# Kernel optimization log

Hardware: AMD Instinct MI355X
Metric: run time of the kernel (lower is better)

## Reference

```python
import jax, jax.numpy as jnp
import numpy as np

IMG_SIZE = 224
ALPHA = 100.0  # hardcoded softmax temperature in knnsearch_t_grad


def _sqdist(a, b):
    # (B,N,C),(B,M,C) -> (B,N,M) squared euclidean distances
    return (jnp.sum(a * a, -1)[:, :, None]
            - 2.0 * jnp.einsum('bnc,bmc->bnm', a, b)
            + jnp.sum(b * b, -1)[:, None, :])


def _cdist(a, b):
    return jnp.sqrt(jnp.maximum(_sqdist(a, b), 1e-12))


def proj2img(pc, img_offset):
    # faithful jax port of GraphDeformLoss_Neural_Partial.proj2img
    B, N, _ = pc.shape
    pc_max = pc.max(axis=1)              # (B,3)
    pc_min_full = pc.min(axis=1)         # (B,3)
    pc_range = pc_max - pc_min_full
    grid_size = pc_range[:, :2].max(axis=-1) / (IMG_SIZE - 3)   # (B,)
    pc_min = pc_min_full[:, None, :2]                            # (B,1,2)
    gs = grid_size[:, None, None]
    idx_xy = jnp.floor((pc[:, :, :2] - pc_min) / gs)             # (B,N,2)
    # densify each point into a 5x5 neighborhood of pixels
    idx_dense = (idx_xy[:, :, None, :] + img_offset[None, None]).reshape(B, N * 25, 2) + 1.0
    center = jnp.floor((idx_dense.max(axis=1) + idx_dense.min(axis=1)) / 2.0)  # (B,2)
    offset = IMG_SIZE / 2.0 - center - 1.0                       # (B,2) = (offset_x, offset_y)
    idx_off = idx_dense + offset[:, None, :]
    # boundary correction as in the torch code, plus clip for safety
    idx_off = idx_off + (idx_off < 0).astype(jnp.float32) - (idx_off > IMG_SIZE - 1).astype(jnp.float32)
    idx_off = jnp.clip(idx_off, 0, IMG_SIZE - 1)
    f_dense = jnp.repeat(jnp.repeat(pc[:, :, None, 2:3], 25, axis=2).reshape(B, N * 25, 1), 3, axis=-1)
    flat = (idx_off[..., 0] * IMG_SIZE + idx_off[..., 1]).astype(jnp.int32)   # (B,N*25)
    out = jax.vmap(lambda f, i: jax.ops.segment_sum(f, i, num_segments=IMG_SIZE * IMG_SIZE))(f_dense, flat)
    img = out.reshape(B, IMG_SIZE, IMG_SIZE, 3).transpose(0, 3, 1, 2)  # (B,3,H,W)
    return jax.nn.sigmoid(img)


def setup_inputs() -> dict:
    key = jax.random.key(0)
    k1, k2, k3, k4 = jax.random.split(key, 4)
    B, N, M, C = 4, 4995, 4995, 128
    off = jnp.array([[i, j] for i in range(-2, 3) for j in range(-2, 3)], dtype=jnp.float32)
    return {
        'verts1': jax.random.normal(k1, (B, N, 3), jnp.float32),
        'verts2': jax.random.normal(k2, (B, M, 3), jnp.float32),
        'feat1': jax.random.normal(k3, (B, N, C), jnp.float32),
        'feat2': jax.random.normal(k4, (B, M, C), jnp.float32),
        'img_offset': off,
        'k': 10,
    }


def reference(verts1, verts2, feat1, feat2, img_offset, k):
    # knnsearch_t_grad: soft correspondence from feature-space cdist + softmax
    d_feat = _cdist(feat1, feat2)                               # (B,N,M)
    Pi_12 = jax.nn.softmax(-ALPHA * d_feat, axis=-1)
    verts12 = jnp.einsum('bnm,bmc->bnc', Pi_12, verts2)         # pulled-back points (B,N,3)
    # chamfer (squared distances, as chamfer_3DDist); partial: take dist1 branch (N<=M)
    d2 = _sqdist(verts12, verts2)
    self_rec_loss = jnp.mean(jnp.min(d2, axis=-1))
    # knn_grad + index_points: gather k-NN features on source cloud
    d2_11 = _sqdist(verts1, verts1)
    _, idx11 = jax.lax.top_k(-d2_11, k)                         # (B,N,k) nearest
    feat1_conv = jax.vmap(lambda p, i: p[i])(feat1, idx11)      # (B,N,k,C)
    deform_feat_loss = jnp.mean((feat1_conv - feat1[:, :, None, :]) ** 2)
    # point-to-image projection loss
    img1 = proj2img(verts12, img_offset)
    img2 = proj2img(verts2, img_offset)
    img_loss = jnp.mean((img1 - img2) ** 2)
    return self_rec_loss + img_loss + deform_feat_loss
```

## Files before the change

### kernel.cpp

```cpp
#include <hip/hip_runtime.h>
#include <math.h>

#define BB 4
#define NN 4995
#define CC 128
#define IMG 224
#define IMGP (IMG*IMG)
#define ALPHA_F 100.0f
#define SPLITS 8
#define COLS_PER_SPLIT 640
#define RBLK 40
#define NG 158
#define NCP 5120
#define NTAP (2*BB*NN*25)
#define NREP 4
#define TKCAP 256

#define SM_SCALE 20813.6898f
#define NEG2S   -41627.3796f
#define EPS_S    2.08136898e-8f

#define OFF_V12    0
#define OFF_FN1    60000
#define OFF_V1Q    81000
#define OFF_V2Q    161000
#define OFF_C2Q    241000
#define OFF_PART   323000
#define OFF_IMG1   1123000
#define OFF_IMG2   1323704
#define OFF_ACC    1524408
#define OFF_STATS  1524792
#define OFF_F2H    1525000
#define OFF_F2L    2820000
#define OFF_IMGR   4115000
#define WS_NEED_REP ((size_t)5721000*sizeof(float))
#define ZERO_START OFF_IMG1
#define ZERO_FLOATS (1524920 - OFF_IMG1)

typedef short v8s  __attribute__((ext_vector_type(8)));
typedef float v16f __attribute__((ext_vector_type(16)));

#if __has_builtin(__builtin_amdgcn_exp2f)
__device__ __forceinline__ float fast_exp2(float x){ return __builtin_amdgcn_exp2f(x); }
#else
__device__ __forceinline__ float fast_exp2(float x){ float r; asm("v_exp_f32 %0, %1" : "=v"(r) : "v"(x)); return r; }
#endif
#if __has_builtin(__builtin_amdgcn_sqrtf)
__device__ __forceinline__ float fast_sqrt(float x){ return __builtin_amdgcn_sqrtf(x); }
#else
__device__ __forceinline__ float fast_sqrt(float x){ float r; asm("v_sqrt_f32 %0, %1" : "=v"(r) : "v"(x)); return r; }
#endif

__device__ __forceinline__ float wave_min(float v){
#pragma unroll
  for (int off=32; off; off>>=1) v = fminf(v, __shfl_xor(v, off));
  return v;
}
__device__ __forceinline__ float wave_sum(float v){
#pragma unroll
  for (int off=32; off; off>>=1) v += __shfl_xor(v, off);
  return v;
}

__device__ __forceinline__ int pack_bf_hi(float a, float b){
  return (int)__builtin_amdgcn_perm(__float_as_uint(b), __float_as_uint(a), 0x07060302u);
}

__device__ __forceinline__ void cvt_hilo(float4 a, float4 c, int4& hi, int4& lo){
  float hx=__uint_as_float(__float_as_uint(a.x)&0xffff0000u);
  float hy=__uint_as_float(__float_as_uint(a.y)&0xffff0000u);
  float hz=__uint_as_float(__float_as_uint(a.z)&0xffff0000u);
  float hw=__uint_as_float(__float_as_uint(a.w)&0xffff0000u);
  float gx=__uint_as_float(__float_as_uint(c.x)&0xffff0000u);
  float gy=__uint_as_float(__float_as_uint(c.y)&0xffff0000u);
  float gz=__uint_as_float(__float_as_uint(c.z)&0xffff0000u);
  float gw=__uint_as_float(__float_as_uint(c.w)&0xffff0000u);
  hi = make_int4(pack_bf_hi(a.x,a.y), pack_bf_hi(a.z,a.w),
                 pack_bf_hi(c.x,c.y), pack_bf_hi(c.z,c.w));
  lo = make_int4(pack_bf_hi(a.x-hx,a.y-hy), pack_bf_hi(a.z-hz,a.w-hw),
                 pack_bf_hi(c.x-gx,c.y-gy), pack_bf_hi(c.z-gz,c.w-gw));
}

__device__ __forceinline__ v8s i4_to_s8(int4 v){
  union { int4 i; v8s s; } u; u.i = v; return u.s;
}

__device__ __forceinline__ void gld_lds16(const void* g, void* l){
  __builtin_amdgcn_global_load_lds((const __attribute__((address_space(1))) void*)g,
                                   (__attribute__((address_space(3))) void*)l, 16, 0, 0);
}

__device__ __forceinline__ unsigned int fkey(float f){
  unsigned int u = __float_as_uint(f);
  return ((int)u < 0) ? ~u : (u ^ 0x80000000u);
}

__global__ __launch_bounds__(256) void k_norms(const float* __restrict__ verts1, const float* __restrict__ verts2,
                        const float* __restrict__ feat1, const float* __restrict__ feat2,
                        float* __restrict__ ws) {
  int gt = blockIdx.x*blockDim.x + threadIdx.x;
  int i = gt >> 2, sub = gt & 3;
  if (i >= BB*NCP) return;
  int b = i / NCP, col = i - b*NCP;
  if (col >= NN){
    if (sub == 0)
      ((float4*)(ws+OFF_C2Q))[i] = make_float4(0.f,0.f,0.f,1e30f);
    return;
  }
  int r = b*NN + col;
  const float4* fa = (const float4*)(feat1 + (size_t)r*CC) + sub*8;
  const float4* fb = (const float4*)(feat2 + (size_t)r*CC) + sub*8;
  float s1=0.f, s2=0.f;
#pragma unroll
  for (int k=0;k<8;k++){
    float4 t = fa[k];
    s1 = fmaf(t.x,t.x,s1); s1 = fmaf(t.y,t.y,s1); s1 = fmaf(t.z,t.z,s1); s1 = fmaf(t.w,t.w,s1);
    float4 u = fb[k];
    s2 = fmaf(u.x,u.x,s2); s2 = fmaf(u.y,u.y,s2); s2 = fmaf(u.z,u.z,s2); s2 = fmaf(u.w,u.w,s2);
  }
  s1 += __shfl_xor(s1,1); s1 += __shfl_xor(s1,2);
  s2 += __shfl_xor(s2,1); s2 += __shfl_xor(s2,2);
  if (sub == 0){
    float x=verts1[(size_t)r*3], y=verts1[(size_t)r*3+1], z=verts1[(size_t)r*3+2];
    ((float4*)(ws+OFF_V1Q))[r] = make_float4(x,y,z, x*x+y*y+z*z);
    float x2=verts2[(size_t)r*3], y2=verts2[(size_t)r*3+1], z2=verts2[(size_t)r*3+2];
    ((float4*)(ws+OFF_V2Q))[r] = make_float4(x2,y2,z2, x2*x2+y2*y2+z2*z2);
    ((float4*)(ws+OFF_C2Q))[i] = make_float4(x2,y2,z2, SM_SCALE*s2);
    ws[OFF_FN1+r] = SM_SCALE*s1;
  }
}

__global__ __launch_bounds__(256) void k_conv(const float* __restrict__ feat2, float* __restrict__ ws) {
  int g = blockIdx.x, b = blockIdx.y;
  int t = threadIdx.x;
  int q = t >> 5, c32 = t & 31;
  int col = g*32 + c32; if (col > NN-1) col = NN-1;
  const float4* src = (const float4*)(feat2 + ((size_t)(b*NN + col))*CC) + q*4;
  float4 v0 = src[0], v1 = src[1], v2 = src[2], v3 = src[3];
  short* f2h = (short*)(ws + OFF_F2H);
  short* f2l = (short*)(ws + OFF_F2L);
  size_t base = ((size_t)(b*NG + g))*4096 + (size_t)q*512 + c32*8;
  int4 hi, lo;
  cvt_hilo(v0, v1, hi, lo);
  *(int4*)&f2h[base] = hi;  *(int4*)&f2l[base] = lo;
  cvt_hilo(v2, v3, hi, lo);
  *(int4*)&f2h[base + 256] = hi;  *(int4*)&f2l[base + 256] = lo;
}

__global__ __launch_bounds__(256) void k_stageA(const float* __restrict__ feat1,
      float* __restrict__ ws) {
  __shared__ __align__(16) short Bbuf[2][4096];

  int rblk  = blockIdx.x;
  int split = blockIdx.y;
  int b     = blockIdx.z;
  int rowBase = rblk*128;
  int colBase = split*COLS_PER_SPLIT;
  int colEnd  = colBase + COLS_PER_SPLIT; if (colEnd > NN) colEnd = NN;
  int nct = (colEnd - colBase + 63) >> 6;
  int nst = nct << 2;

  int t    = threadIdx.x;
  int w    = t >> 6;
  int lane = t & 63;
  int half = lane >> 5;
  int m32  = lane & 31;

  const float* f1b = feat1 + (size_t)b*NN*CC;
  const short* f2h = (const short*)(ws + OFF_F2H);
  const short* f2l = (const short*)(ws + OFF_F2L);
  const float4* cq = (const float4*)(ws + OFF_C2Q) + (size_t)b*NCP + colBase;

  size_t f2base = (((size_t)(b*NG) + (colBase>>5) + (w>>1)) << 12) + (size_t)((t&127)*8);

  {
    short* d = &Bbuf[0][0] + w*512;
    gld_lds16(f2h + f2base, d);
    gld_lds16(f2l + f2base, d + 2048);
  }

  int nrow = rowBase + w*32 + m32;
  int nclamp = nrow > NN-1 ? NN-1 : nrow;
  float sn = ws[OFF_FN1 + (size_t)b*NN + nclamp];
  const float4* ar = (const float4*)(f1b + (size_t)nclamp*CC) + (half<<1);
  v8s Afh[8], Afl[8];
#pragma unroll
  for (int sl=0; sl<8; ++sl){
    float4 v0 = ar[sl*4], v1 = ar[sl*4+1];
    int4 hi, lo;
    cvt_hilo(v0, v1, hi, lo);
    Afh[sl] = i4_to_s8(hi); Afl[sl] = i4_to_s8(lo);
  }

  __syncthreads();

  float mm = INFINITY, S = 0.f, Vx = 0.f, Vy = 0.f, Vz = 0.f;

  for (int ci = 0; ci < nct; ci++){
    v16f acc0, acc1;
#pragma unroll
    for (int i=0;i<16;i++){ acc0[i]=0.f; acc1[i]=0.f; }

#pragma unroll
    for (int kt = 0; kt < 4; kt++){
      int s = (ci<<2) + kt;
      if (s+1 < nst){
        int s1 = s+1;
        size_t so = f2base + ((size_t)(s1>>2)<<13) + ((size_t)(s1&3)<<10);
        short* d = &Bbuf[0][0] + ((s1&1)<<12) + w*512;
        gld_lds16(f2h + so, d);
        gld_lds16(f2l + so, d + 2048);
      }
      const short* Bh = &Bbuf[0][0] + ((s&1)<<12);
      const short* Bl = Bh + 2048;
#pragma unroll
      for (int kh=0; kh<2; kh++){
        int fo = (kh<<9) + (half<<8) + (m32<<3);
        v8s a0h = *(const v8s*)&Bh[fo];
        v8s a0l = *(const v8s*)&Bl[fo];
        v8s a1h = *(const v8s*)&Bh[1024+fo];
        v8s a1l = *(const v8s*)&Bl[1024+fo];
        v8s b1h = Afh[kt*2+kh];
        v8s b1l = Afl[kt*2+kh];
        __builtin_amdgcn_s_setprio(1);
        acc0 = __builtin_amdgcn_mfma_f32_32x32x16_bf16(a0h, b1h, acc0, 0,0,0);
        acc0 = __builtin_amdgcn_mfma_f32_32x32x16_bf16(a0h, b1l, acc0, 0,0,0);
        acc0 = __builtin_amdgcn_mfma_f32_32x32x16_bf16(a0l, b1h, acc0, 0,0,0);
        acc1 = __builtin_amdgcn_mfma_f32_32x32x16_bf16(a1h, b1h, acc1, 0,0,0);
        acc1 = __builtin_amdgcn_mfma_f32_32x32x16_bf16(a1h, b1l, acc1, 0,0,0);
        acc1 = __builtin_amdgcn_mfma_f32_32x32x16_bf16(a1l, b1h, acc1, 0,0,0);
        __builtin_amdgcn_s_setprio(0);
      }
      __syncthreads();
    }

    const float4* cqt = cq + (ci<<6) + (half<<2);
    const float* cqf = (const float*)cqt;
    float Mt = INFINITY;
#pragma unroll
    for (int reg=0; reg<16; reg++){
      int idx = (reg&3) + 8*(reg>>2);
      float f0 = cqf[idx*4 + 3];
      float d0 = fmaf(NEG2S, acc0[reg], sn) + f0;
      float p0 = fast_sqrt(fmaxf(d0, EPS_S));
      acc0[reg] = p0; Mt = fminf(Mt, p0);
      float f1v = cqf[(idx+32)*4 + 3];
      float d1 = fmaf(NEG2S, acc1[reg], sn) + f1v;
      float p1 = fast_sqrt(fmaxf(d1, EPS_S));
      acc1[reg] = p1; Mt = fminf(Mt, p1);
    }
    float mn = fminf(mm, Mt);
    float sc = fast_exp2(mn - mm);
    float se=0.f, sx=0.f, sy=0.f, sz=0.f;
#pragma unroll
    for (int reg=0; reg<16; reg++){
      int idx = (reg&3) + 8*(reg>>2);
      float4 q0 = cqt[idx];
      float e0 = fast_exp2(mn - acc0[reg]);
      se += e0; sx=fmaf(e0,q0.x,sx); sy=fmaf(e0,q0.y,sy); sz=fmaf(e0,q0.z,sz);
      float4 q1 = cqt[idx+32];
      float e1 = fast_exp2(mn - acc1[reg]);
      se += e1; sx=fmaf(e1,q1.x,sx); sy=fmaf(e1,q1.y,sy); sz=fmaf(e1,q1.z,sz);
    }
    S  = fmaf(S,  sc, se);
    Vx = fmaf(Vx, sc, sx);
    Vy = fmaf(Vy, sc, sy);
    Vz = fmaf(Vz, sc, sz);
    mm = mn;
  }

  {
    float m2  = __shfl_xor(mm, 32);
    float S2  = __shfl_xor(S,  32);
    float Vx2 = __shfl_xor(Vx, 32);
    float Vy2 = __shfl_xor(Vy, 32);
    float Vz2 = __shfl_xor(Vz, 32);
    float M = fminf(mm, m2);
    float c1 = fast_exp2(M - mm), c2 = fast_exp2(M - m2);
    float Sf  = S*c1  + S2*c2;
    float Vxf = Vx*c1 + Vx2*c2;
    float Vyf = Vy*c1 + Vy2*c2;
    float Vzf = Vz*c1 + Vz2*c2;
    if (half==0 && nrow < NN){
      float* p = ws + OFF_PART + ((size_t)(b*NN+nrow)*SPLITS + split)*5;
      p[0]=M; p[1]=Sf; p[2]=Vxf; p[3]=Vyf; p[4]=Vzf;
    }
  }
}

__global__ void k_combine(float* __restrict__ ws) {
  int row = blockIdx.x*blockDim.x + threadIdx.x;
  if (row >= BB*NN) return;
  const float* p = ws + OFF_PART + (size_t)row*SPLITS*5;
  float mm = INFINITY;
#pragma unroll
  for (int s=0;s<SPLITS;s++) mm = fminf(mm, p[s*5]);
  float S=0.f,Vx=0.f,Vy=0.f,Vz=0.f;
#pragma unroll
  for (int s=0;s<SPLITS;s++){
    float sc = fast_exp2(mm - p[s*5]);
    S  += p[s*5+1]*sc; Vx += p[s*5+2]*sc; Vy += p[s*5+3]*sc; Vz += p[s*5+4]*sc;
  }
  ws[OFF_V12+(size_t)row*3+0]=Vx/S;
  ws[OFF_V12+(size_t)row*3+1]=Vy/S;
  ws[OFF_V12+(size_t)row*3+2]=Vz/S;
}

__global__ __launch_bounds__(256) void k_selfrec(float* __restrict__ ws) {
  int rblk = blockIdx.x, b = blockIdx.y;
  int lane = threadIdx.x & 63, w = threadIdx.x >> 6;
  int r0 = rblk*32 + w*8;
  const float4* v2q = (const float4*)(ws + OFF_V2Q) + (size_t)b*NN;
  const float* v12 = ws + OFF_V12 + (size_t)b*NN*3;
  float xr[8], yr[8], zr[8], sar[8]; bool val[8];
#pragma unroll
  for (int j=0;j<8;j++){
    int n = r0+j; val[j] = (n < NN); int nc = val[j] ? n : NN-1;
    float x=v12[(size_t)nc*3], y=v12[(size_t)nc*3+1], z=v12[(size_t)nc*3+2];
    sar[j]=x*x+y*y+z*z;
    xr[j]=-2.0f*x; yr[j]=-2.0f*y; zr[j]=-2.0f*z;
  }
  float mn[8];
#pragma unroll
  for (int j=0;j<8;j++) mn[j] = INFINITY;
  for (int m=lane; m<NN; m+=64) {
    float4 q = v2q[m];
#pragma unroll
    for (int j=0;j<8;j++)
      mn[j] = fminf(mn[j], fmaf(xr[j],q.x, fmaf(yr[j],q.y, fmaf(zr[j],q.z, q.w))));
  }
  float s = 0.f;
#pragma unroll
  for (int j=0;j<8;j++){
    float v = wave_min(mn[j]);
    s += val[j] ? (v + sar[j]) : 0.f;
  }
  if (lane==0)
    atomicAdd(((double*)(ws+OFF_ACC)) + ((rblk*4 + w) & 63), (double)s);
}

__global__ __launch_bounds__(256, 4) void k_topk(const float* __restrict__ feat1,
        const int* __restrict__ kptr, float* __restrict__ ws) {
  __shared__ unsigned int keybuf[4*256];
  __shared__ unsigned long long cand[4*TKCAP];
  __shared__ int scnt[4];
  __shared__ float tfs[4];
  __shared__ int sel[4][16];
  __shared__ float rs[4];
  int t = threadIdx.x;
  int lane = t & 63, wid = t >> 6;
  int b = blockIdx.y;
  int n0 = blockIdx.x*4;
  int kk = *kptr; if (kk > 16) kk = 16; if (kk < 1) kk = 1;

  const float4* v1q = (const float4*)(ws + OFF_V1Q) + (size_t)b*NN;
  float mx[4], my2[4], mz[4];
#pragma unroll
  for (int j=0;j<4;j++){
    int n = n0+j; if (n > NN-1) n = NN-1;
    float4 me = v1q[n];
    mx[j]=-2.0f*me.x; my2[j]=-2.0f*me.y; mz[j]=-2.0f*me.z;
  }
  if (t < 4) scnt[t] = 0;

  float e2[20][4];
  float mn[4] = {INFINITY, INFINITY, INFINITY, INFINITY};
#pragma unroll
  for (int i=0;i<19;i++){
    int m = t + 256*i;
    float4 q = v1q[m];
#pragma unroll
    for (int j=0;j<4;j++){
      float d = fmaf(mx[j], q.x, fmaf(my2[j], q.y, fmaf(mz[j], q.z, q.w)));
      e2[i][j] = d; mn[j] = fminf(mn[j], d);
    }
  }
  {
    int m = t + 256*19;
    bool ok = (m < NN);
    float4 q = v1q[ok ? m : NN-1];
#pragma unroll
    for (int j=0;j<4;j++){
      float d = fmaf(mx[j], q.x, fmaf(my2[j], q.y, fmaf(mz[j], q.z, q.w)));
      d = ok ? d : 1e30f;
      e2[19][j] = d; mn[j] = fminf(mn[j], d);
    }
  }

#pragma unroll
  for (int j=0;j<4;j++)
    keybuf[j*256 + t] = fkey(mn[j]) >> 16;
  __syncthreads();

  {
    unsigned int k0 = keybuf[wid*256 + lane];
    unsigned int k1 = keybuf[wid*256 + 64 + lane];
    unsigned int k2 = keybuf[wid*256 + 128 + lane];
    unsigned int k3 = keybuf[wid*256 + 192 + lane];
    unsigned int prefix = 0;
    for (int bit=15; bit>=0; --bit){
      unsigned int piv = prefix | (1u<<bit);
      int c = __popcll(__ballot(k0 < piv)) + __popcll(__ballot(k1 < piv))
            + __popcll(__ballot(k2 < piv)) + __popcll(__ballot(k3 < piv));
      if (c < kk) prefix = piv;
    }
    unsigned int K = (prefix<<16) | 0xFFFFu;
    unsigned int fb = (K & 0x80000000u) ? (K ^ 0x80000000u) : ~K;
    if (lane==0) tfs[wid] = __uint_as_float(fb);
  }
  __syncthreads();
  float tff[4] = {tfs[0], tfs[1], tfs[2], tfs[3]};

#pragma unroll
  for (int i=0;i<20;i++){
    int m = t + 256*i;
#pragma unroll
    for (int j=0;j<4;j++){
      if (e2[i][j] <= tff[j]){
        int pos = atomicAdd(&scnt[j], 1);
        if (pos < TKCAP)
          cand[j*TKCAP + pos] = ((unsigned long long)fkey(e2[i][j]) << 13) | (unsigned int)m;
      }
    }
  }
  __syncthreads();

  {
    int cnt = scnt[wid]; if (cnt > TKCAP) cnt = TKCAP;
    unsigned long long kv0 = (lane       < cnt) ? cand[wid*TKCAP + lane]       : ~0ull;
    unsigned long long kv1 = (lane + 64  < cnt) ? cand[wid*TKCAP + lane + 64]  : ~0ull;
    unsigned long long kv2 = (lane + 128 < cnt) ? cand[wid*TKCAP + lane + 128] : ~0ull;
    unsigned long long kv3 = (lane + 192 < cnt) ? cand[wid*TKCAP + lane + 192] : ~0ull;
    int r0=0, r1=0, r2=0, r3=0;
    for (int q2=0; q2<cnt; ++q2){
      unsigned long long cj = cand[wid*TKCAP + q2];
      r0 += (cj < kv0); r1 += (cj < kv1); r2 += (cj < kv2); r3 += (cj < kv3);
    }
    if (lane       < cnt && r0 < kk) sel[wid][r0] = (int)(kv0 & 8191ull);
    if (lane + 64  < cnt && r1 < kk) sel[wid][r1] = (int)(kv1 & 8191ull);
    if (lane + 128 < cnt && r2 < kk) sel[wid][r2] = (int)(kv2 & 8191ull);
    if (lane + 192 < cnt && r3 < kk) sel[wid][r3] = (int)(kv3 & 8191ull);
  }
  __syncthreads();

  float mse = 0.f;
  int c = t & 127;
  int rh = t >> 7;
  for (int j=0;j<4;j++){
    int n = n0+j;
    if (n >= NN) break;
    const float* f1n = feat1 + ((size_t)b*NN + n)*CC;
    float e = f1n[c];
    for (int r=rh; r<kk; r+=2){
      const float* g = feat1 + ((size_t)b*NN + sel[j][r])*CC;
      float d = g[c]-e;
      mse = fmaf(d,d,mse);
    }
  }

  float acc = wave_sum(mse);
  if (lane==0) rs[wid] = acc;
  __syncthreads();
  if (t==0){
    float s = (rs[0]+rs[1])+(rs[2]+rs[3]);
    atomicAdd(((double*)(ws+OFF_ACC)) + 128 + ((blockIdx.x + b) & 63), (double)s);
  }
}

__global__ void k_imgstats(const float* __restrict__ verts2, const float* __restrict__ imgoff,
                           float* __restrict__ ws) {
  __shared__ float r0[4], r1[4], r2[4], r3[4];
  __shared__ float sgs, smnx, smny;
  int img = blockIdx.x >> 2, b = blockIdx.x & 3;
  const float* pc = (img==0) ? (ws + OFF_V12 + (size_t)b*NN*3) : (verts2 + (size_t)b*NN*3);
  int lane = threadIdx.x & 63, wid = threadIdx.x >> 6;
  float mnx=INFINITY, mxx=-INFINITY, mny=INFINITY, mxy=-INFINITY;
  for (int n = threadIdx.x; n < NN; n += 256) {
    float x = pc[(size_t)n*3], y = pc[(size_t)n*3+1];
    mnx=fminf(mnx,x); mxx=fmaxf(mxx,x); mny=fminf(mny,y); mxy=fmaxf(mxy,y);
  }
#pragma unroll
  for (int off=32; off; off>>=1) {
    mnx=fminf(mnx,__shfl_xor(mnx,off)); mxx=fmaxf(mxx,__shfl_xor(mxx,off));
    mny=fminf(mny,__shfl_xor(mny,off)); mxy=fmaxf(mxy,__shfl_xor(mxy,off));
  }
  if (lane==0){ r0[wid]=mnx; r1[wid]=mxx; r2[wid]=mny; r3[wid]=mxy; }
  __syncthreads();
  float* st = ws + OFF_STATS + (size_t)(img*4+b)*16;
  if (threadIdx.x==0){
    mnx=fminf(fminf(r0[0],r0[1]),fminf(r0[2],r0[3]));
    mxx=fmaxf(fmaxf(r1[0],r1[1]),fmaxf(r1[2],r1[3]));
    mny=fminf(fminf(r2[0],r2[1]),fminf(r2[2],r2[3]));
    mxy=fmaxf(fmaxf(r3[0],r3[1]),fmaxf(r3[2],r3[3]));
    float gs = fmaxf(mxx-mnx, mxy-mny) / 221.0f;
    sgs=gs; smnx=mnx; smny=mny;
    st[0]=mnx; st[1]=mxx; st[2]=mny; st[3]=mxy; st[4]=gs;
  }
  __syncthreads();
  float gs=sgs, bx=smnx, by=smny;
  float fmnx=INFINITY, fmxx=-INFINITY, fmny=INFINITY, fmxy=-INFINITY;
  for (int n = threadIdx.x; n < NN; n += 256) {
    float fx = floorf((pc[(size_t)n*3]-bx)/gs);
    float fy = floorf((pc[(size_t)n*3+1]-by)/gs);
    fmnx=fminf(fmnx,fx); fmxx=fmaxf(fmxx,fx); fmny=fminf(fmny,fy); fmxy=fmaxf(fmxy,fy);
  }
#pragma unroll
  for (int off=32; off; off>>=1) {
    fmnx=fminf(fmnx,__shfl_xor(fmnx,off)); fmxx=fmaxf(fmxx,__shfl_xor(fmxx,off));
    fmny=fminf(fmny,__shfl_xor(fmny,off)); fmxy=fmaxf(fmxy,__shfl_xor(fmxy,off));
  }
  __syncthreads();
  if (lane==0){ r0[wid]=fmnx; r1[wid]=fmxx; r2[wid]=fmny; r3[wid]=fmxy; }
  __syncthreads();
  if (threadIdx.x==0){
    fmnx=fminf(fminf(r0[0],r0[1]),fminf(r0[2],r0[3]));
    fmxx=fmaxf(fmaxf(r1[0],r1[1]),fmaxf(r1[2],r1[3]));
    fmny=fminf(fminf(r2[0],r2[1]),fminf(r2[2],r2[3]));
    fmxy=fmaxf(fmaxf(r3[0],r3[1]),fmaxf(r3[2],r3[3]));
    float omnx=INFINITY, omxx=-INFINITY, omny=INFINITY, omxy=-INFINITY;
    for (int l=0;l<25;l++){
      float ox=imgoff[l*2], oy=imgoff[l*2+1];
      omnx=fminf(omnx,ox); omxx=fmaxf(omxx,ox); omny=fminf(omny,oy); omxy=fmaxf(omxy,oy);
    }
    float cx = floorf(((fmxx+omxx+1.0f)+(fmnx+omnx+1.0f))*0.5f);
    float cy = floorf(((fmxy+omxy+1.0f)+(fmny+omny+1.0f))*0.5f);
    st[5] = (112.0f - cx) - 1.0f;
    st[6] = (112.0f - cy) - 1.0f;
  }
}

__global__ __launch_bounds__(256) void k_scatter(const float* __restrict__ verts2,
                          const float* __restrict__ imgoff,
                          float* __restrict__ ws, int nrep) {
  int g = blockIdx.x*256 + threadIdx.x;
  if (g >= NTAP) return;
  int p = g / 25; int l = g - p*25;
  int img = p / (BB*NN); int r = p - img*(BB*NN); int b = r / NN;
  const float* pc = (img==0) ? (ws + OFF_V12) : verts2;
  float x = pc[(size_t)r*3], y = pc[(size_t)r*3+1], z = pc[(size_t)r*3+2];
  const float* st = ws + OFF_STATS + (size_t)(img*4+b)*16;
  float mnx=st[0], mny=st[2], gs=st[4], offx=st[5], offy=st[6];
  float bx = floorf((x-mnx)/gs) + 1.0f + offx;
  float by = floorf((y-mny)/gs) + 1.0f + offy;
  float vx = bx + imgoff[l*2], vy = by + imgoff[l*2+1];
  vx += (vx<0.f?1.f:0.f) - (vx>223.f?1.f:0.f);
  vy += (vy<0.f?1.f:0.f) - (vy>223.f?1.f:0.f);
  vx = fminf(fmaxf(vx,0.f),223.f); vy = fminf(fmaxf(vy,0.f),223.f);
  int flat = (int)(vx*224.f + vy);
  float* im;
  if (nrep > 1)
    im = ws + OFF_IMGR + ((size_t)(((blockIdx.x & (nrep-1))*2 + img)*BB + b))*IMGP;
  else
    im = ws + (img==0?OFF_IMG1:OFF_IMG2) + (size_t)b*IMGP;
  atomicAdd(im + flat, z);
}

__global__ void k_imgloss(float* __restrict__ ws, int nrep) {
  int i = blockIdx.x*blockDim.x + threadIdx.x;
  float v = 0.f;
  if (i < BB*IMGP) {
    float a, c;
    if (nrep > 1){
      a = 0.f; c = 0.f;
      for (int r=0; r<nrep; ++r){
        a += ws[OFF_IMGR + (size_t)(r*2+0)*BB*IMGP + i];
        c += ws[OFF_IMGR + (size_t)(r*2+1)*BB*IMGP + i];
      }
    } else {
      a = ws[OFF_IMG1+i]; c = ws[OFF_IMG2+i];
    }
    float sa = 1.f/(1.f+expf(-a)), sc = 1.f/(1.f+expf(-c));
    float d = sa - sc; v = d*d;
  }
  v = wave_sum(v);
  if ((threadIdx.x&63)==0)
    atomicAdd(((double*)(ws+OFF_ACC)) + 64 + (blockIdx.x & 63), (double)v);
}

__global__ void k_final(const int* __restrict__ kptr, const float* __restrict__ ws, float* __restrict__ out) {
  const double* acc = (const double*)(ws+OFF_ACC);
  int t = threadIdx.x;
  double a0 = acc[t], a1 = acc[64+t], a2 = acc[128+t];
#pragma unroll
  for (int off=32; off; off>>=1){
    a0 += __shfl_down(a0, off);
    a1 += __shfl_down(a1, off);
    a2 += __shfl_down(a2, off);
  }
  if (t==0){
    int kk = *kptr; if (kk > 16) kk = 16; if (kk < 1) kk = 1;
    double srl = a0 / (double)(BB*NN);
    double img = a1 / ((double)BB*IMGP);
    double df  = a2 / ((double)BB*NN*kk*CC);
    out[0] = (float)(srl + img + df);
  }
}

extern "C" void kernel_launch(void* const* d_in, const int* in_sizes, int n_in,
                              void* d_out, int out_size, void* d_ws, size_t ws_size,
                              hipStream_t stream) {
  (void)in_sizes; (void)n_in; (void)out_size;
  const float* verts1 = (const float*)d_in[0];
  const float* verts2 = (const float*)d_in[1];
  const float* feat1  = (const float*)d_in[2];
  const float* feat2  = (const float*)d_in[3];
  const float* imgoff = (const float*)d_in[4];
  const int*   kptr   = (const int*)d_in[5];
  float* ws  = (float*)d_ws;
  float* out = (float*)d_out;
  int nrep = (ws_size >= WS_NEED_REP) ? NREP : 1;

  hipMemsetAsync(ws + ZERO_START, 0, (size_t)ZERO_FLOATS*sizeof(float), stream);
  if (nrep > 1)
    hipMemsetAsync(ws + OFF_IMGR, 0, (size_t)NREP*2*BB*IMGP*sizeof(float), stream);

  k_norms<<<(BB*NCP*4+255)/256, 256, 0, stream>>>(verts1, verts2, feat1, feat2, ws);

  dim3 gC(NG, BB);
  k_conv<<<gC, 256, 0, stream>>>(feat2, ws);

  dim3 gA(RBLK, SPLITS, BB);
  k_stageA<<<gA, 256, 0, stream>>>(feat1, ws);
  k_combine<<<(BB*NN+255)/256, 256, 0, stream>>>(ws);

  dim3 gS((NN+31)/32, BB);
  k_selfrec<<<gS, 256, 0, stream>>>(ws);

  dim3 gT((NN+3)/4, BB);
  k_topk<<<gT, 256, 0, stream>>>(feat1, kptr, ws);

  k_imgstats<<<8, 256, 0, stream>>>(verts2, imgoff, ws);
  k_scatter<<<(NTAP+255)/256, 256, 0, stream>>>(verts2, imgoff, ws, nrep);
  k_imgloss<<<(BB*IMGP+255)/256, 256, 0, stream>>>(ws, nrep);

  k_final<<<1,64,0,stream>>>(kptr, ws, out);
}
```

Measured before the change: 360.6 us.

## Fuse feat2 norms into conversion, stage column data in LDS, recompute top-k distances

The squared norm of feat2 is now computed inside k_conv from values it already loads, instead of k_norms reading feat2 a second time. k_conv also writes the packed column record (verts2 coordinates plus scaled norm). k_stageA copies each split's column records into shared memory with global_load_lds once, rather than re-reading them from global memory in every tile epilogue. k_topk drops its 80-entry per-thread distance register array and recomputes distances in a second pass, only for threads that can hold a candidate; this lowers register pressure at the cost of reading v1q twice, and its launch-bounds occupancy hint is removed.

```diff
diff --git a/kernel.cpp b/kernel.cpp
--- a/kernel.cpp
+++ b/kernel.cpp
@@ -96,8 +96,7 @@
 }
 
 __global__ __launch_bounds__(256) void k_norms(const float* __restrict__ verts1, const float* __restrict__ verts2,
-                        const float* __restrict__ feat1, const float* __restrict__ feat2,
-                        float* __restrict__ ws) {
+                        const float* __restrict__ feat1, float* __restrict__ ws) {
   int gt = blockIdx.x*blockDim.x + threadIdx.x;
   int i = gt >> 2, sub = gt & 3;
   if (i >= BB*NCP) return;
@@ -109,34 +108,40 @@
   }
   int r = b*NN + col;
   const float4* fa = (const float4*)(feat1 + (size_t)r*CC) + sub*8;
-  const float4* fb = (const float4*)(feat2 + (size_t)r*CC) + sub*8;
-  float s1=0.f, s2=0.f;
+  float s1=0.f;
 #pragma unroll
   for (int k=0;k<8;k++){
     float4 t = fa[k];
     s1 = fmaf(t.x,t.x,s1); s1 = fmaf(t.y,t.y,s1); s1 = fmaf(t.z,t.z,s1); s1 = fmaf(t.w,t.w,s1);
-    float4 u = fb[k];
-    s2 = fmaf(u.x,u.x,s2); s2 = fmaf(u.y,u.y,s2); s2 = fmaf(u.z,u.z,s2); s2 = fmaf(u.w,u.w,s2);
   }
   s1 += __shfl_xor(s1,1); s1 += __shfl_xor(s1,2);
-  s2 += __shfl_xor(s2,1); s2 += __shfl_xor(s2,2);
   if (sub == 0){
     float x=verts1[(size_t)r*3], y=verts1[(size_t)r*3+1], z=verts1[(size_t)r*3+2];
     ((float4*)(ws+OFF_V1Q))[r] = make_float4(x,y,z, x*x+y*y+z*z);
     float x2=verts2[(size_t)r*3], y2=verts2[(size_t)r*3+1], z2=verts2[(size_t)r*3+2];
     ((float4*)(ws+OFF_V2Q))[r] = make_float4(x2,y2,z2, x2*x2+y2*y2+z2*z2);
-    ((float4*)(ws+OFF_C2Q))[i] = make_float4(x2,y2,z2, SM_SCALE*s2);
     ws[OFF_FN1+r] = SM_SCALE*s1;
   }
 }
 
-__global__ __launch_bounds__(256) void k_conv(const float* __restrict__ feat2, float* __restrict__ ws) {
+__global__ __launch_bounds__(256) void k_conv(const float* __restrict__ feat2,
+                                              const float* __restrict__ verts2,
+                                              float* __restrict__ ws) {
+  __shared__ float s2p[8][32];
   int g = blockIdx.x, b = blockIdx.y;
   int t = threadIdx.x;
   int q = t >> 5, c32 = t & 31;
   int col = g*32 + c32; if (col > NN-1) col = NN-1;
   const float4* src = (const float4*)(feat2 + ((size_t)(b*NN + col))*CC) + q*4;
   float4 v0 = src[0], v1 = src[1], v2 = src[2], v3 = src[3];
+  {
+    float s2 = 0.f;
+    s2=fmaf(v0.x,v0.x,s2); s2=fmaf(v0.y,v0.y,s2); s2=fmaf(v0.z,v0.z,s2); s2=fmaf(v0.w,v0.w,s2);
+    s2=fmaf(v1.x,v1.x,s2); s2=fmaf(v1.y,v1.y,s2); s2=fmaf(v1.z,v1.z,s2); s2=fmaf(v1.w,v1.w,s2);
+    s2=fmaf(v2.x,v2.x,s2); s2=fmaf(v2.y,v2.y,s2); s2=fmaf(v2.z,v2.z,s2); s2=fmaf(v2.w,v2.w,s2);
+    s2=fmaf(v3.x,v3.x,s2); s2=fmaf(v3.y,v3.y,s2); s2=fmaf(v3.z,v3.z,s2); s2=fmaf(v3.w,v3.w,s2);
+    s2p[q][c32] = s2;
+  }
   short* f2h = (short*)(ws + OFF_F2H);
   short* f2l = (short*)(ws + OFF_F2L);
   size_t base = ((size_t)(b*NG + g))*4096 + (size_t)q*512 + c32*8;
@@ -145,11 +150,23 @@
   *(int4*)&f2h[base] = hi;  *(int4*)&f2l[base] = lo;
   cvt_hilo(v2, v3, hi, lo);
   *(int4*)&f2h[base + 256] = hi;  *(int4*)&f2l[base + 256] = lo;
+  __syncthreads();
+  if (t < 32){
+    int c = g*32 + t;
+    if (c < NN){
+      float S2 = ((s2p[0][t]+s2p[1][t])+(s2p[2][t]+s2p[3][t]))
+               + ((s2p[4][t]+s2p[5][t])+(s2p[6][t]+s2p[7][t]));
+      size_t r = (size_t)(b*NN + c);
+      float x2=verts2[r*3], y2=verts2[r*3+1], z2=verts2[r*3+2];
+      ((float4*)(ws+OFF_C2Q))[(size_t)b*NCP + c] = make_float4(x2,y2,z2, SM_SCALE*S2);
+    }
+  }
 }
 
 __global__ __launch_bounds__(256) void k_stageA(const float* __restrict__ feat1,
       float* __restrict__ ws) {
   __shared__ __align__(16) short Bbuf[2][4096];
+  __shared__ __align__(16) float colq[768*4];
 
   int rblk  = blockIdx.x;
   int split = blockIdx.y;
@@ -169,7 +186,13 @@
   const float* f1b = feat1 + (size_t)b*NN*CC;
   const short* f2h = (const short*)(ws + OFF_F2H);
   const short* f2l = (const short*)(ws + OFF_F2L);
-  const float4* cq = (const float4*)(ws + OFF_C2Q) + (size_t)b*NCP + colBase;
+  const float4* cqb = (const float4*)(ws + OFF_C2Q) + (size_t)b*NCP;
+
+#pragma unroll
+  for (int r=0; r<3; r++){
+    int col = colBase + r*256 + t; if (col > NCP-1) col = NCP-1;
+    gld_lds16(cqb + col, &colq[(r*256 + w*64)*4]);
+  }
 
   size_t f2base = (((size_t)(b*NG) + (colBase>>5) + (w>>1)) << 12) + (size_t)((t&127)*8);
 
@@ -234,17 +257,16 @@
       __syncthreads();
     }
 
-    const float4* cqt = cq + (ci<<6) + (half<<2);
-    const float* cqf = (const float*)cqt;
+    int cb4 = ci<<8;
     float Mt = INFINITY;
 #pragma unroll
     for (int reg=0; reg<16; reg++){
-      int idx = (reg&3) + 8*(reg>>2);
-      float f0 = cqf[idx*4 + 3];
+      int cp0 = (reg&3) + 8*(reg>>2) + 4*half;
+      float f0 = colq[cb4 + cp0*4 + 3];
       float d0 = fmaf(NEG2S, acc0[reg], sn) + f0;
       float p0 = fast_sqrt(fmaxf(d0, EPS_S));
       acc0[reg] = p0; Mt = fminf(Mt, p0);
-      float f1v = cqf[(idx+32)*4 + 3];
+      float f1v = colq[cb4 + (cp0+32)*4 + 3];
       float d1 = fmaf(NEG2S, acc1[reg], sn) + f1v;
       float p1 = fast_sqrt(fmaxf(d1, EPS_S));
       acc1[reg] = p1; Mt = fminf(Mt, p1);
@@ -254,11 +276,11 @@
     float se=0.f, sx=0.f, sy=0.f, sz=0.f;
 #pragma unroll
     for (int reg=0; reg<16; reg++){
-      int idx = (reg&3) + 8*(reg>>2);
-      float4 q0 = cqt[idx];
+      int cp0 = (reg&3) + 8*(reg>>2) + 4*half;
+      float4 q0 = *(const float4*)&colq[cb4 + cp0*4];
       float e0 = fast_exp2(mn - acc0[reg]);
       se += e0; sx=fmaf(e0,q0.x,sx); sy=fmaf(e0,q0.y,sy); sz=fmaf(e0,q0.z,sz);
-      float4 q1 = cqt[idx+32];
+      float4 q1 = *(const float4*)&colq[cb4 + (cp0+32)*4];
       float e1 = fast_exp2(mn - acc1[reg]);
       se += e1; sx=fmaf(e1,q1.x,sx); sy=fmaf(e1,q1.y,sy); sz=fmaf(e1,q1.z,sz);
     }
@@ -339,7 +361,7 @@
     atomicAdd(((double*)(ws+OFF_ACC)) + ((rblk*4 + w) & 63), (double)s);
 }
 
-__global__ __launch_bounds__(256, 4) void k_topk(const float* __restrict__ feat1,
+__global__ __launch_bounds__(256) void k_topk(const float* __restrict__ feat1,
         const int* __restrict__ kptr, float* __restrict__ ws) {
   __shared__ unsigned int keybuf[4*256];
   __shared__ unsigned long long cand[4*TKCAP];
@@ -363,27 +385,16 @@
   }
   if (t < 4) scnt[t] = 0;
 
-  float e2[20][4];
   float mn[4] = {INFINITY, INFINITY, INFINITY, INFINITY};
-#pragma unroll
-  for (int i=0;i<19;i++){
+  for (int i=0;i<20;i++){
     int m = t + 256*i;
-    float4 q = v1q[m];
-#pragma unroll
-    for (int j=0;j<4;j++){
-      float d = fmaf(mx[j], q.x, fmaf(my2[j], q.y, fmaf(mz[j], q.z, q.w)));
-      e2[i][j] = d; mn[j] = fminf(mn[j], d);
-    }
-  }
-  {
-    int m = t + 256*19;
-    bool ok = (m < NN);
-    float4 q = v1q[ok ? m : NN-1];
-#pragma unroll
-    for (int j=0;j<4;j++){
-      float d = fmaf(mx[j], q.x, fmaf(my2[j], q.y, fmaf(mz[j], q.z, q.w)));
-      d = ok ? d : 1e30f;
-      e2[19][j] = d; mn[j] = fminf(mn[j], d);
+    if (m < NN){
+      float4 q = v1q[m];
+#pragma unroll
+      for (int j=0;j<4;j++){
+        float d = fmaf(mx[j], q.x, fmaf(my2[j], q.y, fmaf(mz[j], q.z, q.w)));
+        mn[j] = fminf(mn[j], d);
+      }
     }
   }
 
@@ -409,17 +420,35 @@
     if (lane==0) tfs[wid] = __uint_as_float(fb);
   }
   __syncthreads();
-  float tff[4] = {tfs[0], tfs[1], tfs[2], tfs[3]};
-
-#pragma unroll
-  for (int i=0;i<20;i++){
-    int m = t + 256*i;
-#pragma unroll
-    for (int j=0;j<4;j++){
-      if (e2[i][j] <= tff[j]){
-        int pos = atomicAdd(&scnt[j], 1);
-        if (pos < TKCAP)
-          cand[j*TKCAP + pos] = ((unsigned long long)fkey(e2[i][j]) << 13) | (unsigned int)m;
+  float tf0 = tfs[0], tf1 = tfs[1], tf2 = tfs[2], tf3 = tfs[3];
+
+  bool g0 = (mn[0] <= tf0), g1 = (mn[1] <= tf1), g2 = (mn[2] <= tf2), g3 = (mn[3] <= tf3);
+  if (g0|g1|g2|g3){
+    for (int i=0;i<20;i++){
+      int m = t + 256*i;
+      if (m < NN){
+        float4 q = v1q[m];
+        float sw = q.w;
+        float d0 = fmaf(mx[0], q.x, fmaf(my2[0], q.y, fmaf(mz[0], q.z, sw)));
+        float d1 = fmaf(mx[1], q.x, fmaf(my2[1], q.y, fmaf(mz[1], q.z, sw)));
+        float d2 = fmaf(mx[2], q.x, fmaf(my2[2], q.y, fmaf(mz[2], q.z, sw)));
+        float d3 = fmaf(mx[3], q.x, fmaf(my2[3], q.y, fmaf(mz[3], q.z, sw)));
+        if (g0 && d0 <= tf0){
+          int pos = atomicAdd(&scnt[0], 1);
+          if (pos < TKCAP) cand[0*TKCAP + pos] = ((unsigned long long)fkey(d0) << 13) | (unsigned int)m;
+        }
+        if (g1 && d1 <= tf1){
+          int pos = atomicAdd(&scnt[1], 1);
+          if (pos < TKCAP) cand[1*TKCAP + pos] = ((unsigned long long)fkey(d1) << 13) | (unsigned int)m;
+        }
+        if (g2 && d2 <= tf2){
+          int pos = atomicAdd(&scnt[2], 1);
+          if (pos < TKCAP) cand[2*TKCAP + pos] = ((unsigned long long)fkey(d2) << 13) | (unsigned int)m;
+        }
+        if (g3 && d3 <= tf3){
+          int pos = atomicAdd(&scnt[3], 1);
+          if (pos < TKCAP) cand[3*TKCAP + pos] = ((unsigned long long)fkey(d3) << 13) | (unsigned int)m;
+        }
       }
     }
   }
@@ -614,10 +643,10 @@
   if (nrep > 1)
     hipMemsetAsync(ws + OFF_IMGR, 0, (size_t)NREP*2*BB*IMGP*sizeof(float), stream);
 
-  k_norms<<<(BB*NCP*4+255)/256, 256, 0, stream>>>(verts1, verts2, feat1, feat2, ws);
+  k_norms<<<(BB*NCP*4+255)/256, 256, 0, stream>>>(verts1, verts2, feat1, ws);
 
   dim3 gC(NG, BB);
-  k_conv<<<gC, 256, 0, stream>>>(feat2, ws);
+  k_conv<<<gC, 256, 0, stream>>>(feat2, verts2, ws);
 
   dim3 gA(RBLK, SPLITS, BB);
   k_stageA<<<gA, 256, 0, stream>>>(feat1, ws);
```

New measurement: 343.1 us. -4.9%, faster.
